# Optimization experiments

Hardware: AMD Instinct MI355X
Metric: run time of the kernel (lower is better)

Reference implementation:

```python
import jax, jax.numpy as jnp
import numpy as np

LEVEL_SHAPES = np.array([[16, 40, 40], [8, 20, 20], [4, 10, 10]], dtype=np.int32)


def _trilinear_sample(vol, grid):
    """Replicates F.grid_sample(mode='bilinear', padding_mode='zeros', align_corners=False).
    vol:  (B, C, T, H, W)
    grid: (B, Q, 3) with last dim (x, y, z) -> indexes (W, H, T), values in [-1, 1]
    returns (B, Q, C)
    """
    B, C, T, H, W = vol.shape
    gx, gy, gz = grid[..., 0], grid[..., 1], grid[..., 2]
    # unnormalize (align_corners=False)
    x = ((gx + 1.0) * W - 1.0) * 0.5
    y = ((gy + 1.0) * H - 1.0) * 0.5
    z = ((gz + 1.0) * T - 1.0) * 0.5
    x0 = jnp.floor(x); y0 = jnp.floor(y); z0 = jnp.floor(z)
    fx = x - x0; fy = y - y0; fz = z - z0
    x0i = x0.astype(jnp.int32); y0i = y0.astype(jnp.int32); z0i = z0.astype(jnp.int32)
    vol_flat = vol.reshape(B, C, T * H * W).transpose(0, 2, 1)  # (B, THW, C)
    out = jnp.zeros(grid.shape[:2] + (C,), dtype=vol.dtype)
    for dz in (0, 1):
        wz = fz if dz else (1.0 - fz)
        zi = z0i + dz
        for dy in (0, 1):
            wy = fy if dy else (1.0 - fy)
            yi = y0i + dy
            for dx in (0, 1):
                wx = fx if dx else (1.0 - fx)
                xi = x0i + dx
                valid = ((xi >= 0) & (xi < W) & (yi >= 0) & (yi < H) & (zi >= 0) & (zi < T))
                idx = jnp.clip((zi * H + yi) * W + xi, 0, T * H * W - 1)
                g = jnp.take_along_axis(vol_flat, idx[..., None], axis=1)  # (B, Q, C)
                out = out + g * (wx * wy * wz * valid.astype(vol.dtype))[..., None]
    return out


def reference(value, value_spatial_shapes, sampling_locations, attention_weights):
    """ms_deform_attn_core_pytorch_3D in jax.
    value: (N, S, M, D); sampling_locations: (N, Lq, M, L, P, 3) in [0,1];
    attention_weights: (N, Lq, M, L, P); returns (N, Lq, M*D)."""
    shapes = np.asarray(value_spatial_shapes)  # static level shapes
    N, S, M, D = value.shape
    _, Lq, _, L, P, _ = sampling_locations.shape
    grids = 2.0 * sampling_locations - 1.0  # (N, Lq, M, L, P, 3)
    sizes = [int(t * h * w) for t, h, w in shapes]
    offs = np.concatenate([[0], np.cumsum(sizes)])
    sampled = []
    for l in range(L):
        T_, H_, W_ = (int(v) for v in shapes[l])
        # (N, THW, M, D) -> (N*M, D, T, H, W)
        v = value[:, offs[l]:offs[l + 1]].transpose(0, 2, 3, 1).reshape(N * M, D, T_, H_, W_)
        # (N, Lq, M, P, 3) -> (N*M, Lq*P, 3)
        g = grids[:, :, :, l].transpose(0, 2, 1, 3, 4).reshape(N * M, Lq * P, 3)
        s = _trilinear_sample(v, g).reshape(N * M, Lq, P, D)
        sampled.append(s)
    sampled = jnp.stack(sampled, axis=2).reshape(N * M, Lq, L * P, D)
    aw = attention_weights.transpose(0, 2, 1, 3, 4).reshape(N * M, Lq, L * P)
    out = jnp.einsum('bqk,bqkd->bqd', aw, sampled)  # (N*M, Lq, D)
    return out.reshape(N, M, Lq, D).transpose(0, 2, 1, 3).reshape(N, Lq, M * D)


def setup_inputs() -> dict:
    key = jax.random.key(0)
    k1, k2, k3 = jax.random.split(key, 3)
    N, M, D = 2, 8, 32
    L, P = 3, 4
    S = int(np.prod(LEVEL_SHAPES, axis=1).sum())  # 29200
    Lq = S
    value = jax.random.normal(k1, (N, S, M, D), dtype=jnp.float32)
    sampling_locations = jax.random.uniform(k2, (N, Lq, M, L, P, 3), dtype=jnp.float32)
    aw = jax.random.normal(k3, (N, Lq, M, L, P), dtype=jnp.float32)
    aw = jax.nn.softmax(aw.reshape(N, Lq, M, L * P), axis=-1).reshape(N, Lq, M, L, P)
    return {
        'value': value,
        'value_spatial_shapes': np.asarray(LEVEL_SHAPES),
        'sampling_locations': sampling_locations,
        'attention_weights': aw,
    }
```

## Files before the change

### kernel.cpp

```cpp
#include <hip/hip_runtime.h>
#include <hip/hip_bf16.h>

typedef float    f32x4 __attribute__((ext_vector_type(4)));
typedef unsigned u32x2 __attribute__((ext_vector_type(2)));
typedef unsigned u32x4 __attribute__((ext_vector_type(4)));

constexpr int kN  = 2;
constexpr int kS  = 29200;
constexpr int kM  = 8;
constexpr int kD  = 32;
constexpr int kL  = 3;
constexpr int kP  = 4;
constexpr int kLq = 29200;

constexpr int kGroups  = 32;
constexpr int kQChunks = (kLq + kGroups - 1) / kGroups;
constexpr int kBlocks  = kN * kM * kQChunks;

constexpr size_t kWsNeed = (size_t)kN * kS * kM * kD * 2;

constexpr int kSlotV = 4;
constexpr int kGrpV  = 12 * kSlotV + 1;
constexpr int kLdsV  = kGroups * kGrpV;

__device__ __forceinline__ f32x4 ntload4(const float* p) {
  return __builtin_nontemporal_load(reinterpret_cast<const f32x4*>(p));
}

__global__ __launch_bounds__(256) void cvtT_kernel(
    const float* __restrict__ in, unsigned short* __restrict__ outb)
{
  const int g     = blockIdx.x * 256 + threadIdx.x;
  const int lane4 = g & 3;
  const int site  = g >> 2;
  const int s  = site % kS;
  const int nm = site / kS;
  const int m  = nm & 7;
  const int n  = nm >> 3;
  const float* ip = in + ((size_t)(n * kS + s) * kM + m) * kD + lane4 * 8;
  const f32x4 a = ntload4(ip);
  const f32x4 b = ntload4(ip + 4);
  unsigned short r[8];
  r[0] = __bfloat16_as_ushort(__float2bfloat16(a[0]));
  r[1] = __bfloat16_as_ushort(__float2bfloat16(a[1]));
  r[2] = __bfloat16_as_ushort(__float2bfloat16(a[2]));
  r[3] = __bfloat16_as_ushort(__float2bfloat16(a[3]));
  r[4] = __bfloat16_as_ushort(__float2bfloat16(b[0]));
  r[5] = __bfloat16_as_ushort(__float2bfloat16(b[1]));
  r[6] = __bfloat16_as_ushort(__float2bfloat16(b[2]));
  r[7] = __bfloat16_as_ushort(__float2bfloat16(b[3]));
  u32x4 pk;
  pk[0] = (unsigned)r[0] | ((unsigned)r[1] << 16);
  pk[1] = (unsigned)r[2] | ((unsigned)r[3] << 16);
  pk[2] = (unsigned)r[4] | ((unsigned)r[5] << 16);
  pk[3] = (unsigned)r[6] | ((unsigned)r[7] << 16);
  *reinterpret_cast<u32x4*>(outb + (size_t)site * kD + lane4 * 8) = pk;
}

__global__ __launch_bounds__(256, 6) void msda3d_bf16_kernel(
    const unsigned short* __restrict__ valb,
    const float* __restrict__ sloc,
    const float* __restrict__ attw,
    float* __restrict__ out)
{
  __shared__ u32x4 lds_v[kLdsV];

  const int bid    = blockIdx.x;
  const int xcd    = bid & 7;
  const int li     = bid >> 3;
  const int half   = (li >= kQChunks) ? 1 : 0;
  const int combo  = xcd * 2 + half;
  const int qblock = li - half * kQChunks;
  const int n = combo >> 3;
  const int m = combo & 7;
  const int tid = threadIdx.x;

  for (int pidx = tid; pidx < 384; pidx += 256) {
    const int pt = pidx >> 5;
    const int g  = pidx & 31;
    const int l  = pt >> 2;
    const int T  = 16 >> l;
    const int H  = 40 >> l;
    const int W  = 40 >> l;
    const int base = (l == 0) ? 0 : ((l == 1) ? 25600 : 28800);

    int q = qblock * kGroups + g;
    if (q >= kLq) q = kLq - 1;
    const size_t qm = (size_t)(n * kLq + q) * kM + m;
    const float gx = sloc[qm * 36 + pt * 3 + 0];
    const float gy = sloc[qm * 36 + pt * 3 + 1];
    const float gz = sloc[qm * 36 + pt * 3 + 2];
    const float aw = attw[qm * 12 + pt];

    const float x = gx * (float)W - 0.5f;
    const float y = gy * (float)H - 0.5f;
    const float z = gz * (float)T - 0.5f;
    const float xf = floorf(x), yf = floorf(y), zf = floorf(z);
    const float fx = x - xf, fy = y - yf, fz = z - zf;
    const int x0 = (int)xf, y0 = (int)yf, z0 = (int)zf;
    const int x1 = x0 + 1, y1 = y0 + 1, z1 = z0 + 1;
    const bool vx0 = (unsigned)x0 < (unsigned)W;
    const bool vx1 = (unsigned)x1 < (unsigned)W;
    const bool vy0 = (unsigned)y0 < (unsigned)H;
    const bool vy1 = (unsigned)y1 < (unsigned)H;
    const bool vz0 = (unsigned)z0 < (unsigned)T;
    const bool vz1 = (unsigned)z1 < (unsigned)T;
    const int xc0 = vx0 ? x0 : 0, xc1 = vx1 ? x1 : 0;
    const int yc0 = vy0 ? y0 : 0, yc1 = vy1 ? y1 : 0;
    const int zc0 = vz0 ? z0 : 0, zc1 = vz1 ? z1 : 0;
    const int r00 = (zc0 * H + yc0) * W;
    const int r01 = (zc0 * H + yc1) * W;
    const int r10 = (zc1 * H + yc0) * W;
    const int r11 = (zc1 * H + yc1) * W;
    const float wx0 = (1.f - fx) * aw, wx1 = fx * aw;
    const float wy0 = 1.f - fy, wy1 = fy;
    const float wz0 = 1.f - fz, wz1 = fz;
    const float w00 = wz0 * wy0, w01 = wz0 * wy1;
    const float w10 = wz1 * wy0, w11 = wz1 * wy1;
    const bool o00 = vz0 && vy0, o01 = vz0 && vy1;
    const bool o10 = vz1 && vy0, o11 = vz1 && vy1;

    u32x4 offA, offB, cwA, cwB;
    offA[0] = (unsigned)(base + r00 + xc0) << 6;
    offA[1] = (unsigned)(base + r00 + xc1) << 6;
    offA[2] = (unsigned)(base + r01 + xc0) << 6;
    offA[3] = (unsigned)(base + r01 + xc1) << 6;
    offB[0] = (unsigned)(base + r10 + xc0) << 6;
    offB[1] = (unsigned)(base + r10 + xc1) << 6;
    offB[2] = (unsigned)(base + r11 + xc0) << 6;
    offB[3] = (unsigned)(base + r11 + xc1) << 6;
    cwA[0] = __float_as_uint((o00 && vx0) ? w00 * wx0 : 0.f);
    cwA[1] = __float_as_uint((o00 && vx1) ? w00 * wx1 : 0.f);
    cwA[2] = __float_as_uint((o01 && vx0) ? w01 * wx0 : 0.f);
    cwA[3] = __float_as_uint((o01 && vx1) ? w01 * wx1 : 0.f);
    cwB[0] = __float_as_uint((o10 && vx0) ? w10 * wx0 : 0.f);
    cwB[1] = __float_as_uint((o10 && vx1) ? w10 * wx1 : 0.f);
    cwB[2] = __float_as_uint((o11 && vx0) ? w11 * wx0 : 0.f);
    cwB[3] = __float_as_uint((o11 && vx1) ? w11 * wx1 : 0.f);

    u32x4* slot = lds_v + g * kGrpV + pt * kSlotV;
    slot[0] = offA;
    slot[1] = offB;
    slot[2] = cwA;
    slot[3] = cwB;
  }
  __syncthreads();

  const int group = tid >> 3;
  const int lane8 = tid & 7;
  const int q = qblock * kGroups + group;

  const char* __restrict__ vbase = reinterpret_cast<const char*>(
      valb + (size_t)combo * kS * kD);
  const unsigned loff = (unsigned)lane8 * 8u;
  const u32x4* slot0 = lds_v + group * kGrpV;

  f32x4 acc = {0.f, 0.f, 0.f, 0.f};

#pragma unroll 1
  for (int pt = 0; pt < 12; ++pt) {
    const u32x4 oA = slot0[pt * kSlotV + 0];
    const u32x4 oB = slot0[pt * kSlotV + 1];
    const u32x4 wA = slot0[pt * kSlotV + 2];
    const u32x4 wB = slot0[pt * kSlotV + 3];

#pragma unroll
    for (int c = 0; c < 8; ++c) {
      const unsigned off = ((c < 4) ? oA[c] : oB[c - 4]) + loff;
      const float w_ = __uint_as_float((c < 4) ? wA[c] : wB[c - 4]);
      const u32x2 v = *reinterpret_cast<const u32x2*>(vbase + off);
      acc[0] = fmaf(__uint_as_float(v[0] << 16),         w_, acc[0]);
      acc[1] = fmaf(__uint_as_float(v[0] & 0xffff0000u), w_, acc[1]);
      acc[2] = fmaf(__uint_as_float(v[1] << 16),         w_, acc[2]);
      acc[3] = fmaf(__uint_as_float(v[1] & 0xffff0000u), w_, acc[3]);
    }
  }

  if (q < kLq) {
    float* __restrict__ op =
        out + (size_t)(n * kLq + q) * (kM * kD) + m * kD + lane8 * 4;
    __builtin_nontemporal_store(acc, reinterpret_cast<f32x4*>(op));
  }
}

__device__ __forceinline__ f32x4 load16f(const float* base, unsigned byteoff) {
  return *reinterpret_cast<const f32x4*>(
      reinterpret_cast<const char*>(base) + byteoff);
}

__global__ __launch_bounds__(256) void msda3d_f32_kernel(
    const float* __restrict__ value,
    const float* __restrict__ sloc,
    const float* __restrict__ attw,
    float* __restrict__ out)
{
  constexpr int LT[3]   = {16, 8, 4};
  constexpr int LH[3]   = {40, 20, 10};
  constexpr int LW[3]   = {40, 20, 10};
  constexpr int LOFF[3] = {0, 25600, 28800};

  const int bid    = blockIdx.x;
  const int xcd    = bid & 7;
  const int li     = bid >> 3;
  const int half   = (li >= kQChunks) ? 1 : 0;
  const int combo  = xcd * 2 + half;
  const int qblock = li - half * kQChunks;
  const int n = combo >> 3;
  const int m = combo & 7;

  const int group = threadIdx.x >> 3;
  const int lane8 = threadIdx.x & 7;
  const int q = qblock * kGroups + group;
  if (q >= kLq) return;

  const size_t qm = (size_t)(n * kLq + q) * kM + m;
  const float* __restrict__ lp = sloc + qm * (kL * kP * 3);
  const float* __restrict__ wp = attw + qm * (kL * kP);
  const float* __restrict__ vbase = value + ((size_t)n * kS * kM + m) * kD;
  const unsigned loff = (unsigned)lane8 * 16u;

  f32x4 acc = {0.f, 0.f, 0.f, 0.f};

#pragma unroll
  for (int l = 0; l < kL; ++l) {
    const int T = LT[l], H = LH[l], W = LW[l];
    const unsigned ubase = ((unsigned)LOFF[l] << 10) + loff;

    const f32x4 c0 = ntload4(lp + l * 12 + 0);
    const f32x4 c1 = ntload4(lp + l * 12 + 4);
    const f32x4 c2 = ntload4(lp + l * 12 + 8);
    const f32x4 w4 = ntload4(wp + l * 4);
    const float crd[12] = {c0[0], c0[1], c0[2], c0[3],
                           c1[0], c1[1], c1[2], c1[3],
                           c2[0], c2[1], c2[2], c2[3]};
    const float aww[4] = {w4[0], w4[1], w4[2], w4[3]};

#pragma unroll
    for (int p = 0; p < kP; ++p) {
      const float gx = crd[p * 3 + 0];
      const float gy = crd[p * 3 + 1];
      const float gz = crd[p * 3 + 2];
      const float aw = aww[p];
      const float x = gx * (float)W - 0.5f;
      const float y = gy * (float)H - 0.5f;
      const float z = gz * (float)T - 0.5f;
      const float xf = floorf(x), yf = floorf(y), zf = floorf(z);
      const float fx = x - xf, fy = y - yf, fz = z - zf;
      const int x0 = (int)xf, y0 = (int)yf, z0 = (int)zf;
      const int x1 = x0 + 1, y1 = y0 + 1, z1 = z0 + 1;
      const bool vx0 = (unsigned)x0 < (unsigned)W;
      const bool vx1 = (unsigned)x1 < (unsigned)W;
      const bool vy0 = (unsigned)y0 < (unsigned)H;
      const bool vy1 = (unsigned)y1 < (unsigned)H;
      const bool vz0 = (unsigned)z0 < (unsigned)T;
      const bool vz1 = (unsigned)z1 < (unsigned)T;
      const int xc0 = vx0 ? x0 : 0, xc1 = vx1 ? x1 : 0;
      const int yc0 = vy0 ? y0 : 0, yc1 = vy1 ? y1 : 0;
      const int zc0 = vz0 ? z0 : 0, zc1 = vz1 ? z1 : 0;
      const int r00 = (zc0 * H + yc0) * W;
      const int r01 = (zc0 * H + yc1) * W;
      const int r10 = (zc1 * H + yc0) * W;
      const int r11 = (zc1 * H + yc1) * W;
      const float wx0 = (1.f - fx) * aw, wx1 = fx * aw;
      const float wy0 = 1.f - fy, wy1 = fy;
      const float wz0 = 1.f - fz, wz1 = fz;
      const float w00 = wz0 * wy0, w01 = wz0 * wy1;
      const float w10 = wz1 * wy0, w11 = wz1 * wy1;
      const bool o00 = vz0 && vy0, o01 = vz0 && vy1;
      const bool o10 = vz1 && vy0, o11 = vz1 && vy1;

      unsigned off[8];
      float cw[8];
      off[0] = ubase + ((unsigned)(r00 + xc0) << 10);
      off[1] = ubase + ((unsigned)(r00 + xc1) << 10);
      off[2] = ubase + ((unsigned)(r01 + xc0) << 10);
      off[3] = ubase + ((unsigned)(r01 + xc1) << 10);
      off[4] = ubase + ((unsigned)(r10 + xc0) << 10);
      off[5] = ubase + ((unsigned)(r10 + xc1) << 10);
      off[6] = ubase + ((unsigned)(r11 + xc0) << 10);
      off[7] = ubase + ((unsigned)(r11 + xc1) << 10);
      cw[0] = (o00 && vx0) ? w00 * wx0 : 0.f;
      cw[1] = (o00 && vx1) ? w00 * wx1 : 0.f;
      cw[2] = (o01 && vx0) ? w01 * wx0 : 0.f;
      cw[3] = (o01 && vx1) ? w01 * wx1 : 0.f;
      cw[4] = (o10 && vx0) ? w10 * wx0 : 0.f;
      cw[5] = (o10 && vx1) ? w10 * wx1 : 0.f;
      cw[6] = (o11 && vx0) ? w11 * wx0 : 0.f;
      cw[7] = (o11 && vx1) ? w11 * wx1 : 0.f;

      f32x4 v[8];
#pragma unroll
      for (int c = 0; c < 8; ++c) v[c] = load16f(vbase, off[c]);
#pragma unroll
      for (int c = 0; c < 8; ++c) acc += v[c] * cw[c];
    }
  }

  float* __restrict__ op =
      out + (size_t)(n * kLq + q) * (kM * kD) + m * kD + lane8 * 4;
  __builtin_nontemporal_store(acc, reinterpret_cast<f32x4*>(op));
}

extern "C" void kernel_launch(void* const* d_in, const int* in_sizes, int n_in,
                              void* d_out, int out_size, void* d_ws, size_t ws_size,
                              hipStream_t stream) {
  const float* value = (const float*)d_in[0];
  const float* sloc  = (const float*)d_in[2];
  const float* attw  = (const float*)d_in[3];
  float* out = (float*)d_out;

  if (ws_size >= kWsNeed) {
    unsigned short* valb = (unsigned short*)d_ws;
    const int nThreads = kN * kM * kS * 4;
    cvtT_kernel<<<nThreads / 256, 256, 0, stream>>>(value, valb);
    msda3d_bf16_kernel<<<kBlocks, 256, 0, stream>>>(valb, sloc, attw, out);
  } else {
    msda3d_f32_kernel<<<kBlocks, 256, 0, stream>>>(value, sloc, attw, out);
  }
}
```

Measured before the change: 203.6 us.

## Fetch adjacent x-corner pairs with 16-byte loads and cross-lane reduce

Each lane now issues one 16-byte load covering 8 channels. The load straddles the x0 and x0+1 sites, reached from an offset biased by +1 site, so 4 row loads replace 8 corner loads per point. Lanes 0-3 apply the x0 weights and lanes 4-7 the x1 weights, and a shuffle-xor reduction merges the halves before the store. The workspace is shifted by 64 bytes so that an x0 of -1 still reads in-bounds padding, and the LDS slot per point shrinks from 4 to 3 vectors. This halves the number of global load instructions and cuts LDS traffic, at the cost of a cross-lane shuffle and wider per-lane loads.

```diff
diff --git a/kernel.cpp b/kernel.cpp
--- a/kernel.cpp
+++ b/kernel.cpp
@@ -2,7 +2,6 @@
 #include <hip/hip_bf16.h>
 
 typedef float    f32x4 __attribute__((ext_vector_type(4)));
-typedef unsigned u32x2 __attribute__((ext_vector_type(2)));
 typedef unsigned u32x4 __attribute__((ext_vector_type(4)));
 
 constexpr int kN  = 2;
@@ -17,9 +16,10 @@
 constexpr int kQChunks = (kLq + kGroups - 1) / kGroups;
 constexpr int kBlocks  = kN * kM * kQChunks;
 
-constexpr size_t kWsNeed = (size_t)kN * kS * kM * kD * 2;
-
-constexpr int kSlotV = 4;
+constexpr size_t kWsData = (size_t)kN * kS * kM * kD * 2;
+constexpr size_t kWsNeed = kWsData + 128;
+
+constexpr int kSlotV = 3;
 constexpr int kGrpV  = 12 * kSlotV + 1;
 constexpr int kLdsV  = kGroups * kGrpV;
 
@@ -58,7 +58,7 @@
 }
 
 __global__ __launch_bounds__(256, 6) void msda3d_bf16_kernel(
-    const unsigned short* __restrict__ valb,
+    const char* __restrict__ wsbase,
     const float* __restrict__ sloc,
     const float* __restrict__ attw,
     float* __restrict__ out)
@@ -105,7 +105,6 @@
     const bool vy1 = (unsigned)y1 < (unsigned)H;
     const bool vz0 = (unsigned)z0 < (unsigned)T;
     const bool vz1 = (unsigned)z1 < (unsigned)T;
-    const int xc0 = vx0 ? x0 : 0, xc1 = vx1 ? x1 : 0;
     const int yc0 = vy0 ? y0 : 0, yc1 = vy1 ? y1 : 0;
     const int zc0 = vz0 ? z0 : 0, zc1 = vz1 ? z1 : 0;
     const int r00 = (zc0 * H + yc0) * W;
@@ -120,29 +119,24 @@
     const bool o00 = vz0 && vy0, o01 = vz0 && vy1;
     const bool o10 = vz1 && vy0, o11 = vz1 && vy1;
 
-    u32x4 offA, offB, cwA, cwB;
-    offA[0] = (unsigned)(base + r00 + xc0) << 6;
-    offA[1] = (unsigned)(base + r00 + xc1) << 6;
-    offA[2] = (unsigned)(base + r01 + xc0) << 6;
-    offA[3] = (unsigned)(base + r01 + xc1) << 6;
-    offB[0] = (unsigned)(base + r10 + xc0) << 6;
-    offB[1] = (unsigned)(base + r10 + xc1) << 6;
-    offB[2] = (unsigned)(base + r11 + xc0) << 6;
-    offB[3] = (unsigned)(base + r11 + xc1) << 6;
-    cwA[0] = __float_as_uint((o00 && vx0) ? w00 * wx0 : 0.f);
-    cwA[1] = __float_as_uint((o00 && vx1) ? w00 * wx1 : 0.f);
-    cwA[2] = __float_as_uint((o01 && vx0) ? w01 * wx0 : 0.f);
-    cwA[3] = __float_as_uint((o01 && vx1) ? w01 * wx1 : 0.f);
-    cwB[0] = __float_as_uint((o10 && vx0) ? w10 * wx0 : 0.f);
-    cwB[1] = __float_as_uint((o10 && vx1) ? w10 * wx1 : 0.f);
-    cwB[2] = __float_as_uint((o11 && vx0) ? w11 * wx0 : 0.f);
-    cwB[3] = __float_as_uint((o11 && vx1) ? w11 * wx1 : 0.f);
+    u32x4 offs, wA, wB;
+    offs[0] = (unsigned)(base + r00 + x0 + 1) << 6;
+    offs[1] = (unsigned)(base + r01 + x0 + 1) << 6;
+    offs[2] = (unsigned)(base + r10 + x0 + 1) << 6;
+    offs[3] = (unsigned)(base + r11 + x0 + 1) << 6;
+    wA[0] = __float_as_uint((o00 && vx0) ? w00 * wx0 : 0.f);
+    wA[1] = __float_as_uint((o01 && vx0) ? w01 * wx0 : 0.f);
+    wA[2] = __float_as_uint((o10 && vx0) ? w10 * wx0 : 0.f);
+    wA[3] = __float_as_uint((o11 && vx0) ? w11 * wx0 : 0.f);
+    wB[0] = __float_as_uint((o00 && vx1) ? w00 * wx1 : 0.f);
+    wB[1] = __float_as_uint((o01 && vx1) ? w01 * wx1 : 0.f);
+    wB[2] = __float_as_uint((o10 && vx1) ? w10 * wx1 : 0.f);
+    wB[3] = __float_as_uint((o11 && vx1) ? w11 * wx1 : 0.f);
 
     u32x4* slot = lds_v + g * kGrpV + pt * kSlotV;
-    slot[0] = offA;
-    slot[1] = offB;
-    slot[2] = cwA;
-    slot[3] = cwB;
+    slot[0] = offs;
+    slot[1] = wA;
+    slot[2] = wB;
   }
   __syncthreads();
 
@@ -150,36 +144,48 @@
   const int lane8 = tid & 7;
   const int q = qblock * kGroups + group;
 
-  const char* __restrict__ vbase = reinterpret_cast<const char*>(
-      valb + (size_t)combo * kS * kD);
-  const unsigned loff = (unsigned)lane8 * 8u;
+  const char* __restrict__ vbase =
+      wsbase + (size_t)combo * (kS * kD * 2);
+  const unsigned loff = (unsigned)lane8 * 16u;
+  const bool hiLane = (lane8 >= 4);
   const u32x4* slot0 = lds_v + group * kGrpV;
 
-  f32x4 acc = {0.f, 0.f, 0.f, 0.f};
+  f32x4 acc0 = {0.f, 0.f, 0.f, 0.f};
+  f32x4 acc1 = {0.f, 0.f, 0.f, 0.f};
 
 #pragma unroll 1
   for (int pt = 0; pt < 12; ++pt) {
-    const u32x4 oA = slot0[pt * kSlotV + 0];
-    const u32x4 oB = slot0[pt * kSlotV + 1];
-    const u32x4 wA = slot0[pt * kSlotV + 2];
-    const u32x4 wB = slot0[pt * kSlotV + 3];
-
-#pragma unroll
-    for (int c = 0; c < 8; ++c) {
-      const unsigned off = ((c < 4) ? oA[c] : oB[c - 4]) + loff;
-      const float w_ = __uint_as_float((c < 4) ? wA[c] : wB[c - 4]);
-      const u32x2 v = *reinterpret_cast<const u32x2*>(vbase + off);
-      acc[0] = fmaf(__uint_as_float(v[0] << 16),         w_, acc[0]);
-      acc[1] = fmaf(__uint_as_float(v[0] & 0xffff0000u), w_, acc[1]);
-      acc[2] = fmaf(__uint_as_float(v[1] << 16),         w_, acc[2]);
-      acc[3] = fmaf(__uint_as_float(v[1] & 0xffff0000u), w_, acc[3]);
+    const u32x4 offs = slot0[pt * kSlotV + 0];
+    const u32x4 wA   = slot0[pt * kSlotV + 1];
+    const u32x4 wB   = slot0[pt * kSlotV + 2];
+
+#pragma unroll
+    for (int i = 0; i < 4; ++i) {
+      const float w_ = __uint_as_float(hiLane ? wB[i] : wA[i]);
+      const u32x4 v = *reinterpret_cast<const u32x4*>(vbase + offs[i] + loff);
+      acc0[0] = fmaf(__uint_as_float(v[0] << 16),         w_, acc0[0]);
+      acc0[1] = fmaf(__uint_as_float(v[0] & 0xffff0000u), w_, acc0[1]);
+      acc0[2] = fmaf(__uint_as_float(v[1] << 16),         w_, acc0[2]);
+      acc0[3] = fmaf(__uint_as_float(v[1] & 0xffff0000u), w_, acc0[3]);
+      acc1[0] = fmaf(__uint_as_float(v[2] << 16),         w_, acc1[0]);
+      acc1[1] = fmaf(__uint_as_float(v[2] & 0xffff0000u), w_, acc1[1]);
+      acc1[2] = fmaf(__uint_as_float(v[3] << 16),         w_, acc1[2]);
+      acc1[3] = fmaf(__uint_as_float(v[3] & 0xffff0000u), w_, acc1[3]);
     }
   }
 
+  f32x4 s0, s1;
+#pragma unroll
+  for (int j = 0; j < 4; ++j) {
+    s0[j] = acc0[j] + __shfl_xor(acc0[j], 4);
+    s1[j] = acc1[j] + __shfl_xor(acc1[j], 4);
+  }
+  const f32x4 stv = hiLane ? s1 : s0;
+
   if (q < kLq) {
-    float* __restrict__ op =
-        out + (size_t)(n * kLq + q) * (kM * kD) + m * kD + lane8 * 4;
-    __builtin_nontemporal_store(acc, reinterpret_cast<f32x4*>(op));
+    float* __restrict__ op = out + (size_t)(n * kLq + q) * (kM * kD) + m * kD +
+                             (lane8 & 3) * 8 + (lane8 >> 2) * 4;
+    __builtin_nontemporal_store(stv, reinterpret_cast<f32x4*>(op));
   }
 }
 
@@ -310,10 +316,11 @@
   float* out = (float*)d_out;
 
   if (ws_size >= kWsNeed) {
-    unsigned short* valb = (unsigned short*)d_ws;
+    unsigned short* valb = (unsigned short*)((char*)d_ws + 64);
     const int nThreads = kN * kM * kS * 4;
     cvtT_kernel<<<nThreads / 256, 256, 0, stream>>>(value, valb);
-    msda3d_bf16_kernel<<<kBlocks, 256, 0, stream>>>(valb, sloc, attw, out);
+    msda3d_bf16_kernel<<<kBlocks, 256, 0, stream>>>(
+        (const char*)d_ws, sloc, attw, out);
   } else {
     msda3d_f32_kernel<<<kBlocks, 256, 0, stream>>>(value, sloc, attw, out);
   }
```

Measured after the change: 164.7 us (median of 2 runs). 19.1% less time.
